# Performance work log

Hardware: AMD Instinct MI355X
Metric: run time of the kernel (lower is better)

## Reference

```python
import jax, jax.numpy as jnp
import numpy as np

B, H, V, T = 32, 1024, 32000, 64

def setup_inputs() -> dict:
    key = jax.random.key(0)
    ks = jax.random.split(key, 8)
    s = 1.0 / np.sqrt(H)
    return {
        "hidden_state": jax.random.normal(ks[0], (1, B, H), jnp.float32),
        "cell_state": jax.random.normal(ks[1], (1, B, H), jnp.float32),
        "W_ih": jax.random.normal(ks[2], (4 * H, H), jnp.float32) * s,
        "W_hh": jax.random.normal(ks[3], (4 * H, H), jnp.float32) * s,
        "b_ih": jax.random.normal(ks[4], (4 * H,), jnp.float32) * s,
        "b_hh": jax.random.normal(ks[5], (4 * H,), jnp.float32) * s,
        "W_out": jax.random.normal(ks[6], (V, H), jnp.float32) * s,
        "b_out": jax.random.normal(ks[7], (V,), jnp.float32) * s,
        "output_len": T,
    }

def reference(hidden_state, cell_state, W_ih, W_hh, b_ih, b_hh, W_out, b_out, output_len):
    h0 = hidden_state[0]  # [B, H]
    c0 = cell_state[0]    # [B, H]
    Hd = h0.shape[-1]
    # Decoder input is all-zeros every step (as in the torch code), so the
    # input-to-hidden contribution reduces to the constant bias b_ih.
    x_gates = jnp.zeros_like(h0) @ W_ih.T + b_ih  # [B, 4H] (keeps W_ih in the graph)

    def step(carry, _):
        h, c = carry
        gates = x_gates + h @ W_hh.T + b_hh  # [B, 4H], torch gate order i,f,g,o
        i, f, g, o = jnp.split(gates, 4, axis=-1)
        c = jax.nn.sigmoid(f) * c + jax.nn.sigmoid(i) * jnp.tanh(g)
        h = jax.nn.sigmoid(o) * jnp.tanh(c)
        logp = jax.nn.log_softmax(h @ W_out.T + b_out, axis=-1)  # [B, V]
        return (h, c), logp

    _, ys = jax.lax.scan(step, (h0, c0), None, length=output_len)  # [T, B, V]
    return jnp.transpose(ys, (1, 0, 2))  # [B, T, V]
```

## Files before the change

kernel.cpp:

```cpp
#include <hip/hip_runtime.h>
#include <hip/hip_bf16.h>
#include <math.h>

#define HD 1024
#define BD 32
#define TD 64
#define VD 32000
#define NWG 128

typedef __attribute__((ext_vector_type(8))) short bf16x8;
typedef __attribute__((ext_vector_type(4))) float f32x4;
typedef __attribute__((ext_vector_type(4))) int i32x4;
typedef unsigned long long u64;

__device__ __forceinline__ short f2bf(float x) {
    __hip_bfloat16 h = __float2bfloat16(x);
    union { __hip_bfloat16 h; short s; } u; u.h = h; return u.s;
}
__device__ __forceinline__ float fsigmoid(float x) {
    return 1.f / (1.f + __expf(-x));
}
__device__ __forceinline__ float ftanh(float x) {
    return 1.f - 2.f / (__expf(2.f * x) + 1.f);
}


__global__ __launch_bounds__(256) void init_kernel(
    const float* __restrict__ Whh_f, const float* __restrict__ bih,
    const float* __restrict__ bhh,  const float* __restrict__ Wout_f,
    const float* __restrict__ h0,
    short* __restrict__ Whh_b, short* __restrict__ Wout_b,
    float* __restrict__ bias,  short* __restrict__ hb, int* __restrict__ ctr)
{
    long i0 = (long)blockIdx.x * blockDim.x + threadIdx.x;
    long stride = (long)gridDim.x * blockDim.x;
    for (long i = i0; i < 20 * TD; i += stride) ctr[i] = 0;
    for (long i = i0; i < (long)VD * HD / 4; i += stride) {
        float4 x = ((const float4*)Wout_f)[i];
        short4 y; y.x = f2bf(x.x); y.y = f2bf(x.y); y.z = f2bf(x.z); y.w = f2bf(x.w);
        ((short4*)Wout_b)[i] = y;
    }
    for (long i = i0; i < (long)4 * HD * HD / 4; i += stride) {
        float4 x = ((const float4*)Whh_f)[i];
        short4 y; y.x = f2bf(x.x); y.y = f2bf(x.y); y.z = f2bf(x.z); y.w = f2bf(x.w);
        ((short4*)Whh_b)[i] = y;
    }
    for (long i = i0; i < 4 * HD; i += stride) bias[i] = bih[i] + bhh[i];
    for (long i = i0; i < BD * HD; i += stride) {
        int b = (int)(i >> 10), j = (int)(i & 1023);
        int kq = j >> 8, ks = (j >> 5) & 7, hi = (j >> 3) & 3, e = j & 7;
        int u = ((kq * 8 + ks) * 2 + (b >> 4)) * 64 + hi * 16 + (b & 15);
        hb[u * 8 + e] = f2bf(h0[i]);
    }
}

__global__ __launch_bounds__(256, 1) void lstm_persist(
    const short* __restrict__ Whh_b,
    const float* __restrict__ bias,
    const float* __restrict__ c0,
    short* __restrict__ hb,
    short* __restrict__ Hmat,
    int* __restrict__ ctrS,
    int* __restrict__ ctrQ)
{
    const int w = blockIdx.x;
    const int tid = threadIdx.x;
    const int kq = tid >> 6;
    const int l = tid & 63;
    const int lo = l & 15, hi = l >> 4;
    const int j0 = w * 8;
    const int kbase = kq * 256 + hi * 8;

    const short* wB0 = Whh_b + (long)((lo >> 3) * HD + j0 + (lo & 7)) * HD + kbase;
    const short* wB1 = Whh_b + (long)(((16 + lo) >> 3) * HD + j0 + ((16 + lo) & 7)) * HD + kbase;
    bf16x8 wb0[8], wb1[8];
    #pragma unroll
    for (int ks = 0; ks < 8; ks++) {
        wb0[ks] = *(const bf16x8*)(wB0 + ks * 32);
        wb1[ks] = *(const bf16x8*)(wB1 + ks * 32);
    }

    const int cb = tid >> 3, cjl = tid & 7;
    float creg = c0[cb * HD + j0 + cjl];
    const float bi  = bias[j0 + cjl];
    const float bf_ = bias[HD + j0 + cjl];
    const float bg  = bias[2 * HD + j0 + cjl];
    const float bo_ = bias[3 * HD + j0 + cjl];

    const int kq0 = w >> 5, ks0 = (w >> 2) & 7, hi0 = w & 3;
    const int sg = (w >> 3) & 3;
    const int ust = ((kq0 * 8 + ks0) * 2 + (cb >> 4)) * 64 + hi0 * 16 + (cb & 15);

    __shared__ float gl[4][32][36];

    for (int t = 0; t < TD; ++t) {
        if (t > 0) {
            const int* cq = &ctrQ[kq * TD + (t - 1)];
            while (__hip_atomic_load(cq, __ATOMIC_RELAXED, __HIP_MEMORY_SCOPE_AGENT) < 4)
                __builtin_amdgcn_s_sleep(1);
        }
        const short* hrb = hb + (size_t)(t & 1) * (BD * HD);

        bf16x8 a0[8], a1[8];
        #pragma unroll
        for (int ks = 0; ks < 8; ks++) {
            const short* p0 = hrb + ((size_t)(((kq * 8 + ks) * 2 + 0) * 64 + l)) * 8;
            const short* p1 = hrb + ((size_t)(((kq * 8 + ks) * 2 + 1) * 64 + l)) * 8;
            asm volatile("global_load_dwordx4 %0, %1, off sc1"
                         : "=v"(a0[ks]) : "v"(p0) : "memory");
            asm volatile("global_load_dwordx4 %0, %1, off sc1"
                         : "=v"(a1[ks]) : "v"(p1) : "memory");
        }
        asm volatile("s_waitcnt vmcnt(0)" ::: "memory");
        __builtin_amdgcn_sched_barrier(0);

        f32x4 acc[2][2] = {};
        #pragma unroll
        for (int ks = 0; ks < 8; ks++) {
            acc[0][0] = __builtin_amdgcn_mfma_f32_16x16x32_bf16(a0[ks], wb0[ks], acc[0][0], 0, 0, 0);
            acc[0][1] = __builtin_amdgcn_mfma_f32_16x16x32_bf16(a0[ks], wb1[ks], acc[0][1], 0, 0, 0);
            acc[1][0] = __builtin_amdgcn_mfma_f32_16x16x32_bf16(a1[ks], wb0[ks], acc[1][0], 0, 0, 0);
            acc[1][1] = __builtin_amdgcn_mfma_f32_16x16x32_bf16(a1[ks], wb1[ks], acc[1][1], 0, 0, 0);
        }
        #pragma unroll
        for (int mf = 0; mf < 2; mf++)
            #pragma unroll
            for (int nf = 0; nf < 2; nf++)
                #pragma unroll
                for (int r = 0; r < 4; r++)
                    gl[kq][mf * 16 + hi * 4 + r][nf * 16 + lo] = acc[mf][nf][r];
        __syncthreads();

        float xi = gl[0][cb][cjl]      + gl[1][cb][cjl]      + gl[2][cb][cjl]      + gl[3][cb][cjl]      + bi;
        float xf = gl[0][cb][8 + cjl]  + gl[1][cb][8 + cjl]  + gl[2][cb][8 + cjl]  + gl[3][cb][8 + cjl]  + bf_;
        float xg = gl[0][cb][16 + cjl] + gl[1][cb][16 + cjl] + gl[2][cb][16 + cjl] + gl[3][cb][16 + cjl] + bg;
        float xo = gl[0][cb][24 + cjl] + gl[1][cb][24 + cjl] + gl[2][cb][24 + cjl] + gl[3][cb][24 + cjl] + bo_;
        float cn = fsigmoid(xf) * creg + fsigmoid(xi) * ftanh(xg);
        float hn = fsigmoid(xo) * ftanh(cn);
        creg = cn;
        short hv = f2bf(hn);
        {
            short* hwb = hb + (size_t)((t + 1) & 1) * (BD * HD);
            unsigned int hval = (unsigned short)hv;
            asm volatile("global_store_short %0, %1, off sc1"
                         :: "v"(hwb + (size_t)ust * 8 + cjl), "v"(hval) : "memory");
        }
        Hmat[((long)cb * TD + t) * HD + j0 + cjl] = hv;
        asm volatile("s_waitcnt vmcnt(0)" ::: "memory");
        __syncthreads();

        if (t < TD - 1 && tid == 0) {
            int old = __hip_atomic_fetch_add(&ctrS[(kq0 * 4 + sg) * TD + t], 1,
                                             __ATOMIC_RELAXED, __HIP_MEMORY_SCOPE_AGENT);
            if (old == 7)
                __hip_atomic_fetch_add(&ctrQ[kq0 * TD + t], 1,
                                       __ATOMIC_RELAXED, __HIP_MEMORY_SCOPE_AGENT);
        }
    }
}

__global__ __launch_bounds__(512, 2) void gemm_logits(
    const short* __restrict__ A,
    const short* __restrict__ Bw,
    const float* __restrict__ bout,
    float* __restrict__ C)
{
    __shared__ short lds[3 * 2048 * 8];
    const int tid = threadIdx.x;
    const int lane = tid & 63, wv = tid >> 6;
    const int lo = lane & 15, hi = lane >> 4;
    const int wm = wv >> 2, wn = wv & 3;
    const long arow0 = (long)blockIdx.x * 256;
    const long brow0 = (long)blockIdx.y * 256;

    const int u0 = tid, u1 = tid + 512;
    const int r0 = (u0 >> 3) * 2 + (u0 & 1);
    const int r1 = (u1 >> 3) * 2 + (u1 & 1);
    const int kc0 = (((u0 & 7) - (r0 & 7)) & 7) >> 1;
    const int kc1 = (((u1 & 7) - (r1 & 7)) & 7) >> 1;
    const short* sA0 = A  + (arow0 + r0) * HD + kc0 * 8;
    const short* sA1 = A  + (arow0 + r1) * HD + kc1 * 8;
    const short* sB0 = Bw + (brow0 + r0) * HD + kc0 * 8;
    const short* sB1 = Bw + (brow0 + r1) * HD + kc1 * 8;

#define STAGE(koff, bb) do { \
    __builtin_amdgcn_global_load_lds((const __attribute__((address_space(1))) short*)(sA0 + (koff)), \
        (__attribute__((address_space(3))) short*)&lds[((bb) + u0) * 8], 16, 0, 0); \
    __builtin_amdgcn_global_load_lds((const __attribute__((address_space(1))) short*)(sA1 + (koff)), \
        (__attribute__((address_space(3))) short*)&lds[((bb) + u1) * 8], 16, 0, 0); \
    __builtin_amdgcn_global_load_lds((const __attribute__((address_space(1))) short*)(sB0 + (koff)), \
        (__attribute__((address_space(3))) short*)&lds[((bb) + 1024 + u0) * 8], 16, 0, 0); \
    __builtin_amdgcn_global_load_lds((const __attribute__((address_space(1))) short*)(sB1 + (koff)), \
        (__attribute__((address_space(3))) short*)&lds[((bb) + 1024 + u1) * 8], 16, 0, 0); \
} while (0)

    int unitA[8], unitB[4];
    #pragma unroll
    for (int mf = 0; mf < 8; mf++) {
        int row = wm * 128 + mf * 16 + lo;
        unitA[mf] = (row >> 1) * 8 + ((2 * hi + (row & 7)) & 7);
    }
    #pragma unroll
    for (int nf = 0; nf < 4; nf++) {
        int row = wn * 64 + nf * 16 + lo;
        unitB[nf] = 1024 + (row >> 1) * 8 + ((2 * hi + (row & 7)) & 7);
    }

    f32x4 acc[8][4] = {};

    STAGE(0, 0);
    STAGE(32, 2048);
    asm volatile("s_waitcnt vmcnt(4)\n\ts_barrier" ::: "memory");

    int br = 0;
    for (int kt = 0; kt < 32; ++kt) {
        int bs = br + 2; if (bs >= 3) bs -= 3;
        int koff = (kt + 2 < 32 ? kt + 2 : 31) * 32;
        STAGE(koff, bs * 2048);

        const int bb = br * 2048;
#define LDF(u) (*(const bf16x8*)&lds[((bb) + (u)) * 8])
        bf16x8 a[8], b[4];
        #pragma unroll
        for (int mf = 0; mf < 4; mf++) a[mf] = LDF(unitA[mf]);
        b[0] = LDF(unitB[0]); b[1] = LDF(unitB[1]);
        __builtin_amdgcn_s_setprio(1);
        #pragma unroll
        for (int mf = 0; mf < 4; mf++) {
            acc[mf][0] = __builtin_amdgcn_mfma_f32_16x16x32_bf16(a[mf], b[0], acc[mf][0], 0, 0, 0);
            acc[mf][1] = __builtin_amdgcn_mfma_f32_16x16x32_bf16(a[mf], b[1], acc[mf][1], 0, 0, 0);
        }
        __builtin_amdgcn_s_setprio(0);
        b[2] = LDF(unitB[2]); b[3] = LDF(unitB[3]);
        __builtin_amdgcn_s_setprio(1);
        #pragma unroll
        for (int mf = 0; mf < 4; mf++) {
            acc[mf][2] = __builtin_amdgcn_mfma_f32_16x16x32_bf16(a[mf], b[2], acc[mf][2], 0, 0, 0);
            acc[mf][3] = __builtin_amdgcn_mfma_f32_16x16x32_bf16(a[mf], b[3], acc[mf][3], 0, 0, 0);
        }
        __builtin_amdgcn_s_setprio(0);
        #pragma unroll
        for (int mf = 4; mf < 8; mf++) a[mf] = LDF(unitA[mf]);
        __builtin_amdgcn_s_setprio(1);
        #pragma unroll
        for (int mf = 4; mf < 8; mf++) {
            acc[mf][2] = __builtin_amdgcn_mfma_f32_16x16x32_bf16(a[mf], b[2], acc[mf][2], 0, 0, 0);
            acc[mf][3] = __builtin_amdgcn_mfma_f32_16x16x32_bf16(a[mf], b[3], acc[mf][3], 0, 0, 0);
        }
        __builtin_amdgcn_s_setprio(0);
        __builtin_amdgcn_s_setprio(1);
        #pragma unroll
        for (int mf = 4; mf < 8; mf++) {
            acc[mf][0] = __builtin_amdgcn_mfma_f32_16x16x32_bf16(a[mf], b[0], acc[mf][0], 0, 0, 0);
            acc[mf][1] = __builtin_amdgcn_mfma_f32_16x16x32_bf16(a[mf], b[1], acc[mf][1], 0, 0, 0);
        }
        __builtin_amdgcn_s_setprio(0);
#undef LDF
        asm volatile("s_waitcnt vmcnt(4)\n\ts_barrier" ::: "memory");
        br = (br + 1 == 3) ? 0 : br + 1;
    }
#undef STAGE

    float bo[4];
    #pragma unroll
    for (int nf = 0; nf < 4; nf++) bo[nf] = bout[brow0 + wn * 64 + nf * 16 + lo];
    #pragma unroll
    for (int mf = 0; mf < 8; mf++)
        #pragma unroll
        for (int r = 0; r < 4; r++) {
            long row = arow0 + wm * 128 + mf * 16 + hi * 4 + r;
            float* cp = C + row * VD + brow0 + wn * 64 + lo;
            #pragma unroll
            for (int nf = 0; nf < 4; nf++)
                cp[nf * 16] = acc[mf][nf][r] + bo[nf];
        }
}

__global__ __launch_bounds__(256) void logsoftmax_inplace(float* __restrict__ C)
{
    const long row = blockIdx.x;
    float* p = C + row * (long)VD;
    const int tid = threadIdx.x;
    float m = -3.4e38f, s = 0.f;
    for (int i = tid; i < VD / 4; i += 256) {
        float4 x = ((const float4*)p)[i];
        float mx = fmaxf(fmaxf(x.x, x.y), fmaxf(x.z, x.w));
        if (mx > m) { s *= __expf(m - mx); m = mx; }
        s += __expf(x.x - m) + __expf(x.y - m) + __expf(x.z - m) + __expf(x.w - m);
    }
    #pragma unroll
    for (int off = 32; off > 0; off >>= 1) {
        float m2 = __shfl_xor(m, off, 64);
        float s2 = __shfl_xor(s, off, 64);
        float mn = fmaxf(m, m2);
        s = s * __expf(m - mn) + s2 * __expf(m2 - mn);
        m = mn;
    }
    __shared__ float sm[4], ss[4];
    if ((tid & 63) == 0) { sm[tid >> 6] = m; ss[tid >> 6] = s; }
    __syncthreads();
    float M = fmaxf(fmaxf(sm[0], sm[1]), fmaxf(sm[2], sm[3]));
    float S = ss[0] * __expf(sm[0] - M) + ss[1] * __expf(sm[1] - M) +
              ss[2] * __expf(sm[2] - M) + ss[3] * __expf(sm[3] - M);
    float lse = M + logf(S);
    for (int i = tid; i < VD / 4; i += 256) {
        float4 x = ((float4*)p)[i];
        x.x -= lse; x.y -= lse; x.z -= lse; x.w -= lse;
        ((float4*)p)[i] = x;
    }
}

extern "C" void kernel_launch(void* const* d_in, const int* in_sizes, int n_in,
                              void* d_out, int out_size, void* d_ws, size_t ws_size,
                              hipStream_t stream)
{
    const float* h0   = (const float*)d_in[0];
    const float* c0   = (const float*)d_in[1];
    const float* Whh  = (const float*)d_in[3];
    const float* bih  = (const float*)d_in[4];
    const float* bhh  = (const float*)d_in[5];
    const float* Wout = (const float*)d_in[6];
    const float* bout = (const float*)d_in[7];

    char* ws = (char*)d_ws;
    short* Wout_b = (short*)ws;  ws += (size_t)VD * HD * 2;
    short* Whh_b  = (short*)ws;  ws += (size_t)4 * HD * HD * 2;
    short* Hmat   = (short*)ws;  ws += (size_t)BD * TD * HD * 2;
    short* hb     = (short*)ws;  ws += (size_t)2 * BD * HD * 2;
    float* bias   = (float*)ws;  ws += (size_t)4 * HD * 4;
    int*   ctr    = (int*)ws;    ws += 20 * TD * sizeof(int);
    float* C      = (float*)d_out;

    int* ctrS = ctr;
    int* ctrQ = ctr + 16 * TD;

    init_kernel<<<2048, 256, 0, stream>>>(Whh, bih, bhh, Wout, h0,
                                          Whh_b, Wout_b, bias, hb, ctr);
    lstm_persist<<<NWG, 256, 0, stream>>>(Whh_b, bias, c0, hb, Hmat, ctrS, ctrQ);
    gemm_logits<<<dim3(8, 125), 512, 0, stream>>>(Hmat, Wout_b, bout, C);
    logsoftmax_inplace<<<2048, 256, 0, stream>>>(C);
}
```

Measured before the change: 571.6 us.

## Fuse LSTM recurrence and logits GEMM into one persistent kernel with work queue

Merges the persistent LSTM kernel and the output-projection GEMM into a single launch. Extra workgroups pull 128x128 GEMM tiles from an atomic queue and spin on the per-timestep counters until the needed hidden states exist, so logits for early timesteps are computed while the recurrence is still running. Hmat is reordered to time-major and the GEMM tile shrinks to 128x128 with 256 threads and double buffering. The risks are contention between GEMM and LSTM workgroups for compute units and bandwidth, which could slow the latency-bound recurrence, and possible deadlock if the LSTM workgroups are not all resident at once.

```diff
diff --git a/kernel.cpp b/kernel.cpp
--- a/kernel.cpp
+++ b/kernel.cpp
@@ -7,11 +7,12 @@
 #define TD 64
 #define VD 32000
 #define NWG 128
+#define GW  512
+#define NTM 16
+#define NTN 250
 
 typedef __attribute__((ext_vector_type(8))) short bf16x8;
 typedef __attribute__((ext_vector_type(4))) float f32x4;
-typedef __attribute__((ext_vector_type(4))) int i32x4;
-typedef unsigned long long u64;
 
 __device__ __forceinline__ short f2bf(float x) {
     __hip_bfloat16 h = __float2bfloat16(x);
@@ -34,7 +35,7 @@
 {
     long i0 = (long)blockIdx.x * blockDim.x + threadIdx.x;
     long stride = (long)gridDim.x * blockDim.x;
-    for (long i = i0; i < 20 * TD; i += stride) ctr[i] = 0;
+    for (long i = i0; i < 21 * TD; i += stride) ctr[i] = 0;
     for (long i = i0; i < (long)VD * HD / 4; i += stride) {
         float4 x = ((const float4*)Wout_f)[i];
         short4 y; y.x = f2bf(x.x); y.y = f2bf(x.y); y.z = f2bf(x.z); y.w = f2bf(x.w);
@@ -54,226 +55,221 @@
     }
 }
 
-__global__ __launch_bounds__(256, 1) void lstm_persist(
+__global__ __launch_bounds__(256, 2) void fused_lstm_gemm(
     const short* __restrict__ Whh_b,
     const float* __restrict__ bias,
     const float* __restrict__ c0,
     short* __restrict__ hb,
     short* __restrict__ Hmat,
+    const short* __restrict__ Bw,
+    const float* __restrict__ bout,
+    float* __restrict__ C,
     int* __restrict__ ctrS,
-    int* __restrict__ ctrQ)
+    int* __restrict__ ctrQ,
+    int* __restrict__ queue)
 {
-    const int w = blockIdx.x;
+    __shared__ alignas(16) char shmem[32768];
+    __shared__ int tau_sh;
     const int tid = threadIdx.x;
-    const int kq = tid >> 6;
-    const int l = tid & 63;
-    const int lo = l & 15, hi = l >> 4;
-    const int j0 = w * 8;
-    const int kbase = kq * 256 + hi * 8;
-
-    const short* wB0 = Whh_b + (long)((lo >> 3) * HD + j0 + (lo & 7)) * HD + kbase;
-    const short* wB1 = Whh_b + (long)(((16 + lo) >> 3) * HD + j0 + ((16 + lo) & 7)) * HD + kbase;
-    bf16x8 wb0[8], wb1[8];
-    #pragma unroll
-    for (int ks = 0; ks < 8; ks++) {
-        wb0[ks] = *(const bf16x8*)(wB0 + ks * 32);
-        wb1[ks] = *(const bf16x8*)(wB1 + ks * 32);
-    }
-
-    const int cb = tid >> 3, cjl = tid & 7;
-    float creg = c0[cb * HD + j0 + cjl];
-    const float bi  = bias[j0 + cjl];
-    const float bf_ = bias[HD + j0 + cjl];
-    const float bg  = bias[2 * HD + j0 + cjl];
-    const float bo_ = bias[3 * HD + j0 + cjl];
-
-    const int kq0 = w >> 5, ks0 = (w >> 2) & 7, hi0 = w & 3;
-    const int sg = (w >> 3) & 3;
-    const int ust = ((kq0 * 8 + ks0) * 2 + (cb >> 4)) * 64 + hi0 * 16 + (cb & 15);
-
-    __shared__ float gl[4][32][36];
-
-    for (int t = 0; t < TD; ++t) {
-        if (t > 0) {
-            const int* cq = &ctrQ[kq * TD + (t - 1)];
-            while (__hip_atomic_load(cq, __ATOMIC_RELAXED, __HIP_MEMORY_SCOPE_AGENT) < 4)
-                __builtin_amdgcn_s_sleep(1);
-        }
-        const short* hrb = hb + (size_t)(t & 1) * (BD * HD);
-
-        bf16x8 a0[8], a1[8];
+
+    if (blockIdx.x < NWG) {
+        float (*gl)[32][36] = (float (*)[32][36])shmem;
+        const int w = blockIdx.x;
+        const int kq = tid >> 6;
+        const int l = tid & 63;
+        const int lo = l & 15, hi = l >> 4;
+        const int j0 = w * 8;
+        const int kbase = kq * 256 + hi * 8;
+
+        const short* wB0 = Whh_b + (long)((lo >> 3) * HD + j0 + (lo & 7)) * HD + kbase;
+        const short* wB1 = Whh_b + (long)(((16 + lo) >> 3) * HD + j0 + ((16 + lo) & 7)) * HD + kbase;
+        bf16x8 wb0[8], wb1[8];
         #pragma unroll
         for (int ks = 0; ks < 8; ks++) {
-            const short* p0 = hrb + ((size_t)(((kq * 8 + ks) * 2 + 0) * 64 + l)) * 8;
-            const short* p1 = hrb + ((size_t)(((kq * 8 + ks) * 2 + 1) * 64 + l)) * 8;
-            asm volatile("global_load_dwordx4 %0, %1, off sc1"
-                         : "=v"(a0[ks]) : "v"(p0) : "memory");
-            asm volatile("global_load_dwordx4 %0, %1, off sc1"
-                         : "=v"(a1[ks]) : "v"(p1) : "memory");
-        }
-        asm volatile("s_waitcnt vmcnt(0)" ::: "memory");
-        __builtin_amdgcn_sched_barrier(0);
-
-        f32x4 acc[2][2] = {};
-        #pragma unroll
-        for (int ks = 0; ks < 8; ks++) {
-            acc[0][0] = __builtin_amdgcn_mfma_f32_16x16x32_bf16(a0[ks], wb0[ks], acc[0][0], 0, 0, 0);
-            acc[0][1] = __builtin_amdgcn_mfma_f32_16x16x32_bf16(a0[ks], wb1[ks], acc[0][1], 0, 0, 0);
-            acc[1][0] = __builtin_amdgcn_mfma_f32_16x16x32_bf16(a1[ks], wb0[ks], acc[1][0], 0, 0, 0);
-            acc[1][1] = __builtin_amdgcn_mfma_f32_16x16x32_bf16(a1[ks], wb1[ks], acc[1][1], 0, 0, 0);
-        }
-        #pragma unroll
-        for (int mf = 0; mf < 2; mf++)
-            #pragma unroll
-            for (int nf = 0; nf < 2; nf++)
-                #pragma unroll
-                for (int r = 0; r < 4; r++)
-                    gl[kq][mf * 16 + hi * 4 + r][nf * 16 + lo] = acc[mf][nf][r];
-        __syncthreads();
-
-        float xi = gl[0][cb][cjl]      + gl[1][cb][cjl]      + gl[2][cb][cjl]      + gl[3][cb][cjl]      + bi;
-        float xf = gl[0][cb][8 + cjl]  + gl[1][cb][8 + cjl]  + gl[2][cb][8 + cjl]  + gl[3][cb][8 + cjl]  + bf_;
-        float xg = gl[0][cb][16 + cjl] + gl[1][cb][16 + cjl] + gl[2][cb][16 + cjl] + gl[3][cb][16 + cjl] + bg;
-        float xo = gl[0][cb][24 + cjl] + gl[1][cb][24 + cjl] + gl[2][cb][24 + cjl] + gl[3][cb][24 + cjl] + bo_;
-        float cn = fsigmoid(xf) * creg + fsigmoid(xi) * ftanh(xg);
-        float hn = fsigmoid(xo) * ftanh(cn);
-        creg = cn;
-        short hv = f2bf(hn);
-        {
-            short* hwb = hb + (size_t)((t + 1) & 1) * (BD * HD);
-            unsigned int hval = (unsigned short)hv;
-            asm volatile("global_store_short %0, %1, off sc1"
-                         :: "v"(hwb + (size_t)ust * 8 + cjl), "v"(hval) : "memory");
-        }
-        Hmat[((long)cb * TD + t) * HD + j0 + cjl] = hv;
-        asm volatile("s_waitcnt vmcnt(0)" ::: "memory");
-        __syncthreads();
-
-        if (t < TD - 1 && tid == 0) {
-            int old = __hip_atomic_fetch_add(&ctrS[(kq0 * 4 + sg) * TD + t], 1,
-                                             __ATOMIC_RELAXED, __HIP_MEMORY_SCOPE_AGENT);
-            if (old == 7)
-                __hip_atomic_fetch_add(&ctrQ[kq0 * TD + t], 1,
-                                       __ATOMIC_RELAXED, __HIP_MEMORY_SCOPE_AGENT);
-        }
-    }
-}
-
-__global__ __launch_bounds__(512, 2) void gemm_logits(
-    const short* __restrict__ A,
-    const short* __restrict__ Bw,
-    const float* __restrict__ bout,
-    float* __restrict__ C)
-{
-    __shared__ short lds[3 * 2048 * 8];
-    const int tid = threadIdx.x;
-    const int lane = tid & 63, wv = tid >> 6;
-    const int lo = lane & 15, hi = lane >> 4;
-    const int wm = wv >> 2, wn = wv & 3;
-    const long arow0 = (long)blockIdx.x * 256;
-    const long brow0 = (long)blockIdx.y * 256;
-
-    const int u0 = tid, u1 = tid + 512;
-    const int r0 = (u0 >> 3) * 2 + (u0 & 1);
-    const int r1 = (u1 >> 3) * 2 + (u1 & 1);
-    const int kc0 = (((u0 & 7) - (r0 & 7)) & 7) >> 1;
-    const int kc1 = (((u1 & 7) - (r1 & 7)) & 7) >> 1;
-    const short* sA0 = A  + (arow0 + r0) * HD + kc0 * 8;
-    const short* sA1 = A  + (arow0 + r1) * HD + kc1 * 8;
-    const short* sB0 = Bw + (brow0 + r0) * HD + kc0 * 8;
-    const short* sB1 = Bw + (brow0 + r1) * HD + kc1 * 8;
-
-#define STAGE(koff, bb) do { \
-    __builtin_amdgcn_global_load_lds((const __attribute__((address_space(1))) short*)(sA0 + (koff)), \
-        (__attribute__((address_space(3))) short*)&lds[((bb) + u0) * 8], 16, 0, 0); \
-    __builtin_amdgcn_global_load_lds((const __attribute__((address_space(1))) short*)(sA1 + (koff)), \
-        (__attribute__((address_space(3))) short*)&lds[((bb) + u1) * 8], 16, 0, 0); \
-    __builtin_amdgcn_global_load_lds((const __attribute__((address_space(1))) short*)(sB0 + (koff)), \
-        (__attribute__((address_space(3))) short*)&lds[((bb) + 1024 + u0) * 8], 16, 0, 0); \
-    __builtin_amdgcn_global_load_lds((const __attribute__((address_space(1))) short*)(sB1 + (koff)), \
-        (__attribute__((address_space(3))) short*)&lds[((bb) + 1024 + u1) * 8], 16, 0, 0); \
-} while (0)
-
-    int unitA[8], unitB[4];
-    #pragma unroll
-    for (int mf = 0; mf < 8; mf++) {
-        int row = wm * 128 + mf * 16 + lo;
-        unitA[mf] = (row >> 1) * 8 + ((2 * hi + (row & 7)) & 7);
-    }
-    #pragma unroll
-    for (int nf = 0; nf < 4; nf++) {
-        int row = wn * 64 + nf * 16 + lo;
-        unitB[nf] = 1024 + (row >> 1) * 8 + ((2 * hi + (row & 7)) & 7);
-    }
-
-    f32x4 acc[8][4] = {};
-
-    STAGE(0, 0);
-    STAGE(32, 2048);
-    asm volatile("s_waitcnt vmcnt(4)\n\ts_barrier" ::: "memory");
-
-    int br = 0;
-    for (int kt = 0; kt < 32; ++kt) {
-        int bs = br + 2; if (bs >= 3) bs -= 3;
-        int koff = (kt + 2 < 32 ? kt + 2 : 31) * 32;
-        STAGE(koff, bs * 2048);
-
-        const int bb = br * 2048;
-#define LDF(u) (*(const bf16x8*)&lds[((bb) + (u)) * 8])
-        bf16x8 a[8], b[4];
-        #pragma unroll
-        for (int mf = 0; mf < 4; mf++) a[mf] = LDF(unitA[mf]);
-        b[0] = LDF(unitB[0]); b[1] = LDF(unitB[1]);
-        __builtin_amdgcn_s_setprio(1);
+            wb0[ks] = *(const bf16x8*)(wB0 + ks * 32);
+            wb1[ks] = *(const bf16x8*)(wB1 + ks * 32);
+        }
+
+        const int cb = tid >> 3, cjl = tid & 7;
+        float creg = c0[cb * HD + j0 + cjl];
+        const float bi  = bias[j0 + cjl];
+        const float bf_ = bias[HD + j0 + cjl];
+        const float bg  = bias[2 * HD + j0 + cjl];
+        const float bo_ = bias[3 * HD + j0 + cjl];
+
+        const int kq0 = w >> 5, ks0 = (w >> 2) & 7, hi0 = w & 3;
+        const int sg = (w >> 3) & 3;
+        const int ust = ((kq0 * 8 + ks0) * 2 + (cb >> 4)) * 64 + hi0 * 16 + (cb & 15);
+
+        for (int t = 0; t < TD; ++t) {
+            if (t > 0) {
+                const int* cq = &ctrQ[kq * TD + (t - 1)];
+                while (__hip_atomic_load(cq, __ATOMIC_RELAXED, __HIP_MEMORY_SCOPE_AGENT) < 4)
+                    __builtin_amdgcn_s_sleep(1);
+            }
+            const short* hrb = hb + (size_t)(t & 1) * (BD * HD);
+
+            bf16x8 a0[8], a1[8];
+            #pragma unroll
+            for (int ks = 0; ks < 8; ks++) {
+                const short* p0 = hrb + ((size_t)(((kq * 8 + ks) * 2 + 0) * 64 + l)) * 8;
+                const short* p1 = hrb + ((size_t)(((kq * 8 + ks) * 2 + 1) * 64 + l)) * 8;
+                asm volatile("global_load_dwordx4 %0, %1, off sc1"
+                             : "=v"(a0[ks]) : "v"(p0) : "memory");
+                asm volatile("global_load_dwordx4 %0, %1, off sc1"
+                             : "=v"(a1[ks]) : "v"(p1) : "memory");
+            }
+            asm volatile("s_waitcnt vmcnt(0)" ::: "memory");
+            __builtin_amdgcn_sched_barrier(0);
+
+            f32x4 acc[2][2] = {};
+            #pragma unroll
+            for (int ks = 0; ks < 8; ks++) {
+                acc[0][0] = __builtin_amdgcn_mfma_f32_16x16x32_bf16(a0[ks], wb0[ks], acc[0][0], 0, 0, 0);
+                acc[0][1] = __builtin_amdgcn_mfma_f32_16x16x32_bf16(a0[ks], wb1[ks], acc[0][1], 0, 0, 0);
+                acc[1][0] = __builtin_amdgcn_mfma_f32_16x16x32_bf16(a1[ks], wb0[ks], acc[1][0], 0, 0, 0);
+                acc[1][1] = __builtin_amdgcn_mfma_f32_16x16x32_bf16(a1[ks], wb1[ks], acc[1][1], 0, 0, 0);
+            }
+            #pragma unroll
+            for (int mf = 0; mf < 2; mf++)
+                #pragma unroll
+                for (int nf = 0; nf < 2; nf++)
+                    #pragma unroll
+                    for (int r = 0; r < 4; r++)
+                        gl[kq][mf * 16 + hi * 4 + r][nf * 16 + lo] = acc[mf][nf][r];
+            __syncthreads();
+
+            float xi = gl[0][cb][cjl]      + gl[1][cb][cjl]      + gl[2][cb][cjl]      + gl[3][cb][cjl]      + bi;
+            float xf = gl[0][cb][8 + cjl]  + gl[1][cb][8 + cjl]  + gl[2][cb][8 + cjl]  + gl[3][cb][8 + cjl]  + bf_;
+            float xg = gl[0][cb][16 + cjl] + gl[1][cb][16 + cjl] + gl[2][cb][16 + cjl] + gl[3][cb][16 + cjl] + bg;
+            float xo = gl[0][cb][24 + cjl] + gl[1][cb][24 + cjl] + gl[2][cb][24 + cjl] + gl[3][cb][24 + cjl] + bo_;
+            float cn = fsigmoid(xf) * creg + fsigmoid(xi) * ftanh(xg);
+            float hn = fsigmoid(xo) * ftanh(cn);
+            creg = cn;
+            short hv = f2bf(hn);
+            {
+                unsigned int hval = (unsigned short)hv;
+                short* hm  = Hmat + ((size_t)t * BD + cb) * HD + j0 + cjl;
+                short* hwb = hb + (size_t)((t + 1) & 1) * (BD * HD) + (size_t)ust * 8 + cjl;
+                asm volatile("global_store_short %0, %1, off sc1" :: "v"(hm),  "v"(hval) : "memory");
+                asm volatile("global_store_short %0, %1, off sc1" :: "v"(hwb), "v"(hval) : "memory");
+            }
+            asm volatile("s_waitcnt vmcnt(0)" ::: "memory");
+            __syncthreads();
+
+            if (tid == 0) {
+                int old = __hip_atomic_fetch_add(&ctrS[(kq0 * 4 + sg) * TD + t], 1,
+                                                 __ATOMIC_RELAXED, __HIP_MEMORY_SCOPE_AGENT);
+                if (old == 7)
+                    __hip_atomic_fetch_add(&ctrQ[kq0 * TD + t], 1,
+                                           __ATOMIC_RELAXED, __HIP_MEMORY_SCOPE_AGENT);
+            }
+        }
+    } else {
+        short* lds = (short*)shmem;
+        const int lane = tid & 63, wv = tid >> 6;
+        const int lo = lane & 15, hi = lane >> 4;
+        const int wm = wv >> 1, wn = wv & 1;
+
+        const int u0 = tid, u1 = tid + 256;
+        const int r0 = (u0 >> 3) * 2 + (u0 & 1);
+        const int r1 = (u1 >> 3) * 2 + (u1 & 1);
+        const int kc0 = (((u0 & 7) - (r0 & 7)) & 7) >> 1;
+        const int kc1 = (((u1 & 7) - (r1 & 7)) & 7) >> 1;
+
+        int unitA[4], unitB[4];
         #pragma unroll
         for (int mf = 0; mf < 4; mf++) {
-            acc[mf][0] = __builtin_amdgcn_mfma_f32_16x16x32_bf16(a[mf], b[0], acc[mf][0], 0, 0, 0);
-            acc[mf][1] = __builtin_amdgcn_mfma_f32_16x16x32_bf16(a[mf], b[1], acc[mf][1], 0, 0, 0);
-        }
-        __builtin_amdgcn_s_setprio(0);
-        b[2] = LDF(unitB[2]); b[3] = LDF(unitB[3]);
-        __builtin_amdgcn_s_setprio(1);
+            int row = wm * 64 + mf * 16 + lo;
+            unitA[mf] = (row >> 1) * 8 + ((2 * hi + (row & 7)) & 7);
+        }
         #pragma unroll
-        for (int mf = 0; mf < 4; mf++) {
-            acc[mf][2] = __builtin_amdgcn_mfma_f32_16x16x32_bf16(a[mf], b[2], acc[mf][2], 0, 0, 0);
-            acc[mf][3] = __builtin_amdgcn_mfma_f32_16x16x32_bf16(a[mf], b[3], acc[mf][3], 0, 0, 0);
-        }
-        __builtin_amdgcn_s_setprio(0);
-        #pragma unroll
-        for (int mf = 4; mf < 8; mf++) a[mf] = LDF(unitA[mf]);
-        __builtin_amdgcn_s_setprio(1);
-        #pragma unroll
-        for (int mf = 4; mf < 8; mf++) {
-            acc[mf][2] = __builtin_amdgcn_mfma_f32_16x16x32_bf16(a[mf], b[2], acc[mf][2], 0, 0, 0);
-            acc[mf][3] = __builtin_amdgcn_mfma_f32_16x16x32_bf16(a[mf], b[3], acc[mf][3], 0, 0, 0);
-        }
-        __builtin_amdgcn_s_setprio(0);
-        __builtin_amdgcn_s_setprio(1);
-        #pragma unroll
-        for (int mf = 4; mf < 8; mf++) {
-            acc[mf][0] = __builtin_amdgcn_mfma_f32_16x16x32_bf16(a[mf], b[0], acc[mf][0], 0, 0, 0);
-            acc[mf][1] = __builtin_amdgcn_mfma_f32_16x16x32_bf16(a[mf], b[1], acc[mf][1], 0, 0, 0);
-        }
-        __builtin_amdgcn_s_setprio(0);
-#undef LDF
-        asm volatile("s_waitcnt vmcnt(4)\n\ts_barrier" ::: "memory");
-        br = (br + 1 == 3) ? 0 : br + 1;
-    }
-#undef STAGE
-
-    float bo[4];
-    #pragma unroll
-    for (int nf = 0; nf < 4; nf++) bo[nf] = bout[brow0 + wn * 64 + nf * 16 + lo];
-    #pragma unroll
-    for (int mf = 0; mf < 8; mf++)
-        #pragma unroll
-        for (int r = 0; r < 4; r++) {
-            long row = arow0 + wm * 128 + mf * 16 + hi * 4 + r;
-            float* cp = C + row * VD + brow0 + wn * 64 + lo;
-            #pragma unroll
-            for (int nf = 0; nf < 4; nf++)
-                cp[nf * 16] = acc[mf][nf][r] + bo[nf];
-        }
+        for (int nf = 0; nf < 4; nf++) {
+            int row = wn * 64 + nf * 16 + lo;
+            unitB[nf] = 512 + (row >> 1) * 8 + ((2 * hi + (row & 7)) & 7);
+        }
+
+        for (;;) {
+            if (tid == 0)
+                tau_sh = __hip_atomic_fetch_add(queue, 1, __ATOMIC_RELAXED, __HIP_MEMORY_SCOPE_AGENT);
+            __syncthreads();
+            int tau = tau_sh;
+            if (tau >= NTM * NTN) break;
+            int m = tau / NTN, n = tau - m * NTN;
+
+            if (tid == 0) {
+                int tr = m * 4 + 3;
+                #pragma unroll
+                for (int q = 0; q < 4; q++)
+                    while (__hip_atomic_load(&ctrQ[q * TD + tr], __ATOMIC_RELAXED,
+                                             __HIP_MEMORY_SCOPE_AGENT) < 4)
+                        __builtin_amdgcn_s_sleep(8);
+            }
+            __syncthreads();
+
+            const short* pA0 = Hmat + ((long)m * 128 + r0) * HD + kc0 * 8;
+            const short* pA1 = Hmat + ((long)m * 128 + r1) * HD + kc1 * 8;
+            const short* pB0 = Bw + ((long)n * 128 + r0) * HD + kc0 * 8;
+            const short* pB1 = Bw + ((long)n * 128 + r1) * HD + kc1 * 8;
+
+#define GSTAGE(koff, bb) do { \
+    __builtin_amdgcn_global_load_lds((const __attribute__((address_space(1))) short*)(pA0 + (koff)), \
+        (__attribute__((address_space(3))) short*)&lds[((bb) + u0) * 8], 16, 0, 0); \
+    __builtin_amdgcn_global_load_lds((const __attribute__((address_space(1))) short*)(pA1 + (koff)), \
+        (__attribute__((address_space(3))) short*)&lds[((bb) + u1) * 8], 16, 0, 0); \
+    __builtin_amdgcn_global_load_lds((const __attribute__((address_space(1))) short*)(pB0 + (koff)), \
+        (__attribute__((address_space(3))) short*)&lds[((bb) + 512 + u0) * 8], 16, 0, 0); \
+    __builtin_amdgcn_global_load_lds((const __attribute__((address_space(1))) short*)(pB1 + (koff)), \
+        (__attribute__((address_space(3))) short*)&lds[((bb) + 512 + u1) * 8], 16, 0, 0); \
+} while (0)
+
+            f32x4 acc[4][4] = {};
+            GSTAGE(0, 0);
+            GSTAGE(32, 1024);
+            asm volatile("s_waitcnt vmcnt(4)\n\ts_barrier" ::: "memory");
+
+            for (int kt = 0; kt < 32; ++kt) {
+                const int bb = (kt & 1) * 1024;
+                bf16x8 a[4], b[4];
+                #pragma unroll
+                for (int mf = 0; mf < 4; mf++) a[mf] = *(const bf16x8*)&lds[(bb + unitA[mf]) * 8];
+                #pragma unroll
+                for (int nf = 0; nf < 4; nf++) b[nf] = *(const bf16x8*)&lds[(bb + unitB[nf]) * 8];
+                __builtin_amdgcn_s_setprio(1);
+                #pragma unroll
+                for (int mf = 0; mf < 4; mf++)
+                    #pragma unroll
+                    for (int nf = 0; nf < 4; nf++)
+                        acc[mf][nf] = __builtin_amdgcn_mfma_f32_16x16x32_bf16(a[mf], b[nf], acc[mf][nf], 0, 0, 0);
+                __builtin_amdgcn_s_setprio(0);
+                __builtin_amdgcn_s_barrier();
+                if (kt + 2 < 32) {
+                    GSTAGE((kt + 2) * 32, bb);
+                    asm volatile("s_waitcnt vmcnt(4)" ::: "memory");
+                } else {
+                    asm volatile("s_waitcnt vmcnt(0)" ::: "memory");
+                }
+                __builtin_amdgcn_s_barrier();
+            }
+#undef GSTAGE
+
+            float bo[4];
+            #pragma unroll
+            for (int nf = 0; nf < 4; nf++) bo[nf] = bout[n * 128 + wn * 64 + nf * 16 + lo];
+            #pragma unroll
+            for (int mf = 0; mf < 4; mf++)
+                #pragma unroll
+                for (int r = 0; r < 4; r++) {
+                    int trow = m * 128 + wm * 64 + mf * 16 + hi * 4 + r;
+                    int bt = trow & 31, tt = trow >> 5;
+                    float* cp = C + ((long)bt * TD + tt) * VD + n * 128 + wn * 64 + lo;
+                    #pragma unroll
+                    for (int nf = 0; nf < 4; nf++)
+                        cp[nf * 16] = acc[mf][nf][r] + bo[nf];
+                }
+            __syncthreads();
+        }
+    }
 }
 
 __global__ __launch_bounds__(256) void logsoftmax_inplace(float* __restrict__ C)
@@ -328,15 +324,16 @@
     short* Hmat   = (short*)ws;  ws += (size_t)BD * TD * HD * 2;
     short* hb     = (short*)ws;  ws += (size_t)2 * BD * HD * 2;
     float* bias   = (float*)ws;  ws += (size_t)4 * HD * 4;
-    int*   ctr    = (int*)ws;    ws += 20 * TD * sizeof(int);
+    int*   ctr    = (int*)ws;    ws += 21 * TD * sizeof(int);
     float* C      = (float*)d_out;
 
-    int* ctrS = ctr;
-    int* ctrQ = ctr + 16 * TD;
+    int* ctrS  = ctr;
+    int* ctrQ  = ctr + 16 * TD;
+    int* queue = ctr + 20 * TD;
 
     init_kernel<<<2048, 256, 0, stream>>>(Whh, bih, bhh, Wout, h0,
                                           Whh_b, Wout_b, bias, hb, ctr);
-    lstm_persist<<<NWG, 256, 0, stream>>>(Whh_b, bias, c0, hb, Hmat, ctrS, ctrQ);
-    gemm_logits<<<dim3(8, 125), 512, 0, stream>>>(Hmat, Wout_b, bout, C);
+    fused_lstm_gemm<<<NWG + GW, 256, 0, stream>>>(Whh_b, bias, c0, hb, Hmat,
+                                                  Wout_b, bout, C, ctrS, ctrQ, queue);
     logsoftmax_inplace<<<2048, 256, 0, stream>>>(C);
 }
```

After: 502.1 us. 1.14x faster.
